# Kernel optimization log

Measured on AMD Instinct MI355X. Metric: run time of the kernel, lower is better.

Reference implementation:

```python
import jax, jax.numpy as jnp
import numpy as np

B, S, H = 2, 1024, 1024
NH, HD = 8, 128
E, TOPK, MI = 8, 2, 1024
SI = 2 * MI  # shared experts intermediate (n_shared_experts=2)
EPS = 1e-6
THETA = 10000.0


def setup_inputs() -> dict:
    key = jax.random.key(0)
    ks = jax.random.split(key, 16)
    w = lambda k, shp: (0.02 * jax.random.normal(k, shp, dtype=jnp.float32))
    # RoPE tables [S, HD]
    inv_freq = 1.0 / (THETA ** (np.arange(0, HD, 2, dtype=np.float32) / HD))
    t = np.arange(S, dtype=np.float32)
    freqs = np.outer(t, inv_freq)
    emb = np.concatenate([freqs, freqs], axis=-1)
    return {
        "hidden_states": jax.random.normal(ks[0], (B, S, H), dtype=jnp.float32),
        "ln1_w": jnp.ones((H,), jnp.float32),
        "ln2_w": jnp.ones((H,), jnp.float32),
        "q_w": w(ks[1], (H, H)),
        "k_w": w(ks[2], (H, H)),
        "v_w": w(ks[3], (H, H)),
        "o_w": w(ks[4], (H, H)),
        "cos": jnp.asarray(np.cos(emb), jnp.float32),
        "sin": jnp.asarray(np.sin(emb), jnp.float32),
        "gate_w": w(ks[5], (E, H)),
        "eg_w": w(ks[6], (E, MI, H)),
        "eu_w": w(ks[7], (E, MI, H)),
        "ed_w": w(ks[8], (E, H, MI)),
        "sg_w": w(ks[9], (SI, H)),
        "su_w": w(ks[10], (SI, H)),
        "sd_w": w(ks[11], (H, SI)),
    }


def _rmsnorm(x, w):
    return x * jax.lax.rsqrt(jnp.mean(x * x, axis=-1, keepdims=True) + EPS) * w


def _rotate_half(x):
    x1, x2 = jnp.split(x, 2, axis=-1)
    return jnp.concatenate([-x2, x1], axis=-1)


def _attention(x, q_w, k_w, v_w, o_w, cos, sin):
    b, s, h = x.shape
    q = (x @ q_w.T).reshape(b, s, NH, HD)
    k = (x @ k_w.T).reshape(b, s, NH, HD)
    v = (x @ v_w.T).reshape(b, s, NH, HD)
    c = cos[None, :s, None, :]
    sn = sin[None, :s, None, :]
    q = q * c + _rotate_half(q) * sn
    k = k * c + _rotate_half(k) * sn
    scores = jnp.einsum("bqhd,bkhd->bhqk", q, k) / jnp.sqrt(jnp.float32(HD))
    causal = jnp.tril(jnp.ones((s, s), dtype=bool))
    scores = jnp.where(causal[None, None], scores, -jnp.inf)
    p = jax.nn.softmax(scores, axis=-1)
    out = jnp.einsum("bhqk,bkhd->bqhd", p, v).reshape(b, s, h)
    return out @ o_w.T


def _mlp(x, gw, uw, dw):
    return (jax.nn.silu(x @ gw.T) * (x @ uw.T)) @ dw.T


def _moe(x, gate_w, eg_w, eu_w, ed_w, sg_w, su_w, sd_w):
    b, s, h = x.shape
    xt = x.reshape(-1, h)                              # [T, H]
    T = xt.shape[0]
    probs = jax.nn.softmax(xt @ gate_w.T, axis=-1)     # [T, E]
    rw, idx = jax.lax.top_k(probs, TOPK)               # [T, K]
    rw = rw / (jnp.sum(rw, axis=-1, keepdims=True) + 1e-20)  # norm_topk_prob
    # dense combine weights [T, E] (zero for unselected experts)
    w_full = jnp.zeros((T, E), xt.dtype).at[jnp.arange(T)[:, None], idx].add(rw)
    # dense all-expert compute, masked-combined (faithful to per-token loop math)
    g = jax.nn.silu(jnp.einsum("th,eih->tei", xt, eg_w))
    u = jnp.einsum("th,eih->tei", xt, eu_w)
    y = jnp.einsum("tei,ehi->teh", g * u, ed_w)        # [T, E, H]
    routed = jnp.einsum("teh,te->th", y, w_full)
    shared = _mlp(xt, sg_w, su_w, sd_w)
    return (routed + shared).reshape(b, s, h)


def reference(hidden_states, ln1_w, ln2_w, q_w, k_w, v_w, o_w, cos, sin,
              gate_w, eg_w, eu_w, ed_w, sg_w, su_w, sd_w):
    x = hidden_states
    x = x + _attention(_rmsnorm(x, ln1_w), q_w, k_w, v_w, o_w, cos, sin)
    x = x + _moe(_rmsnorm(x, ln2_w), gate_w, eg_w, eu_w, ed_w, sg_w, su_w, sd_w)
    return x
```

## Files before the change

kernel.cpp:

```cpp
#include <hip/hip_runtime.h>

#define B_   2
#define S_   1024
#define H_   1024
#define NH_  8
#define HD_  128
#define E_   8
#define MI_  1024
#define SI_  2048
#define T_   2048
#define CAP_ 2048

typedef unsigned short u16;
typedef __attribute__((ext_vector_type(4))) float f32x4;
typedef __attribute__((ext_vector_type(4))) unsigned short u16x4;
typedef __attribute__((ext_vector_type(8))) unsigned short u16x8;
typedef __attribute__((ext_vector_type(8))) __bf16 bf16x8;

__device__ __forceinline__ u16 f2bf(float f) {
  unsigned int u = __builtin_bit_cast(unsigned int, f);
  u = (u + 0x7fffu + ((u >> 16) & 1u)) >> 16;
  return (u16)u;
}
__device__ __forceinline__ float bf2f(u16 u) {
  return __builtin_bit_cast(float, (unsigned int)u << 16);
}
__device__ __forceinline__ float wave_sum(float v) {
#pragma unroll
  for (int o = 32; o; o >>= 1) v += __shfl_down(v, o, 64);
  return v;
}
__device__ __forceinline__ void gll16(const u16* g, u16* l) {
  __builtin_amdgcn_global_load_lds((const __attribute__((address_space(1))) void*)g,
                                   (__attribute__((address_space(3))) void*)l, 16, 0, 0);
}

__global__ void cvt_all(const float* __restrict__ q_w, const float* __restrict__ k_w,
                        const float* __restrict__ v_w, const float* __restrict__ o_w,
                        const float* __restrict__ eg_w, const float* __restrict__ eu_w,
                        const float* __restrict__ ed_w, const float* __restrict__ sg_w,
                        const float* __restrict__ su_w, const float* __restrict__ sd_w,
                        u16* __restrict__ qwb, u16* __restrict__ egu, u16* __restrict__ edb,
                        u16* __restrict__ sgu, u16* __restrict__ sdb,
                        const float* __restrict__ hidden, const float* __restrict__ ln1w,
                        u16* __restrict__ xn) {
  int bid = blockIdx.x, tid = threadIdx.x;
  if (bid >= 4352) {
    int t = bid - 4352;
    f32x4 v = ((const f32x4*)(hidden + (long)t * H_))[tid];
    float ss = v[0]*v[0] + v[1]*v[1] + v[2]*v[2] + v[3]*v[3];
    __shared__ float red[4];
    float s = wave_sum(ss);
    if ((tid & 63) == 0) red[tid >> 6] = s;
    __syncthreads();
    float r = rsqrtf((red[0] + red[1] + red[2] + red[3]) * (1.0f / H_) + 1e-6f);
    f32x4 wv = ((const f32x4*)ln1w)[tid];
    u16x4 o;
#pragma unroll
    for (int c = 0; c < 4; c++) o[c] = f2bf(v[c] * r * wv[c]);
    ((u16x4*)(xn + (long)t * H_))[tid] = o;
    return;
  }
  const float* src[8];
  u16* dst[8];
#pragma unroll
  for (int g = 0; g < 8; g++) {
    int row = bid * 8 + g;
    if (row < 4096) {
      int seg = row >> 10;
      const float* in = (seg == 0) ? q_w : (seg == 1) ? k_w : (seg == 2) ? v_w : o_w;
      src[g] = in + (long)(row & 1023) * 1024;
      dst[g] = qwb + (long)row * 1024;
    } else if (row < 20480) {
      int rel = row - 4096;
      int zu = rel >= 8192;
      int r = rel & 8191;
      int e = r >> 10, i = r & 1023;
      int orow = (i >> 4) * 32 + (i & 15) + (zu ? 16 : 0);
      src[g] = (zu ? eu_w : eg_w) + (long)r * 1024;
      dst[g] = egu + ((long)e * 2048 + orow) * 1024;
    } else if (row < 28672) {
      long f = (long)(row - 20480) * 1024;
      src[g] = ed_w + f;
      dst[g] = edb + f;
    } else if (row < 32768) {
      int rel = row - 28672;
      int zu = rel >= 2048;
      int i = rel & 2047;
      int orow = (i >> 4) * 32 + (i & 15) + (zu ? 16 : 0);
      src[g] = (zu ? su_w : sg_w) + (long)i * 1024;
      dst[g] = sgu + (long)orow * 1024;
    } else {
      long f = (long)(row - 32768) * 1024;
      src[g] = sd_w + f;
      dst[g] = sdb + f;
    }
  }
  f32x4 v[8];
#pragma unroll
  for (int g = 0; g < 8; g++)
    v[g] = __builtin_nontemporal_load((const f32x4*)src[g] + tid);
#pragma unroll
  for (int g = 0; g < 8; g++) {
    u16x4 o;
#pragma unroll
    for (int c = 0; c < 4; c++) o[c] = f2bf(v[g][c]);
    ((u16x4*)dst[g])[tid] = o;
  }
}

__global__ void rmsnorm2_gate(const float* __restrict__ x1, const float* __restrict__ ln2w,
                              const float* __restrict__ gw, u16* __restrict__ xn,
                              int* __restrict__ eidx, float* __restrict__ aw) {
  int t = blockIdx.x, tid = threadIdx.x;
  int lane = tid & 63, wave = tid >> 6;
  f32x4 v = ((const f32x4*)(x1 + (long)t * H_))[tid];
  float ss = v[0]*v[0] + v[1]*v[1] + v[2]*v[2] + v[3]*v[3];
  __shared__ float redS[4];
  __shared__ float redE[4][E_];
  float s = wave_sum(ss);
  if (lane == 0) redS[wave] = s;
  __syncthreads();
  float r = rsqrtf((redS[0] + redS[1] + redS[2] + redS[3]) * (1.0f / H_) + 1e-6f);
  f32x4 wv = ((const f32x4*)ln2w)[tid];
  float xv[4];
  u16x4 o;
#pragma unroll
  for (int c = 0; c < 4; c++) { xv[c] = v[c] * r * wv[c]; o[c] = f2bf(xv[c]); }
  ((u16x4*)(xn + (long)t * H_))[tid] = o;
  float acc[E_];
#pragma unroll
  for (int e = 0; e < E_; e++) {
    f32x4 g = ((const f32x4*)(gw + (long)e * H_))[tid];
    acc[e] = xv[0]*g[0] + xv[1]*g[1] + xv[2]*g[2] + xv[3]*g[3];
  }
#pragma unroll
  for (int e = 0; e < E_; e++) acc[e] = wave_sum(acc[e]);
  if (lane == 0)
#pragma unroll
    for (int e = 0; e < E_; e++) redE[wave][e] = acc[e];
  __syncthreads();
  if (tid == 0) {
    float l[E_];
#pragma unroll
    for (int e = 0; e < E_; e++) l[e] = redE[0][e] + redE[1][e] + redE[2][e] + redE[3][e];
    float mx = l[0];
#pragma unroll
    for (int e = 1; e < E_; e++) mx = fmaxf(mx, l[e]);
    float p[E_], z = 0.f;
#pragma unroll
    for (int e = 0; e < E_; e++) { p[e] = __expf(l[e] - mx); z += p[e]; }
    int e0 = 0;
#pragma unroll
    for (int e = 1; e < E_; e++) if (p[e] > p[e0]) e0 = e;
    int e1 = (e0 == 0) ? 1 : 0;
#pragma unroll
    for (int e = 0; e < E_; e++) if (e != e0 && p[e] > p[e1]) e1 = e;
    float q0 = p[e0] / z, q1 = p[e1] / z;
    float invs = 1.0f / (q0 + q1 + 1e-20f);
    eidx[t * 2] = e0;
    eidx[t * 2 + 1] = e1;
    aw[t * 2] = q0 * invs;
    aw[t * 2 + 1] = q1 * invs;
  }
}

__global__ __launch_bounds__(256) void route_scan(const int* __restrict__ eidx,
                                                  int* __restrict__ arow,
                                                  int* __restrict__ cursor,
                                                  int* __restrict__ itok,
                                                  int* __restrict__ wlist) {
  __shared__ int sc[E_][256];
  int tid = threadIdx.x;
  unsigned c0 = 0, c1 = 0;
  int ebuf[16];
#pragma unroll
  for (int i = 0; i < 16; i++) {
    int e = eidx[tid * 16 + i];
    ebuf[i] = e;
    if (e < 4) c0 += 1u << (8 * e); else c1 += 1u << (8 * (e - 4));
  }
#pragma unroll
  for (int e = 0; e < E_; e++)
    sc[e][tid] = (e < 4) ? (int)((c0 >> (8 * e)) & 0xff) : (int)((c1 >> (8 * (e - 4))) & 0xff);
  __syncthreads();
  for (int st = 1; st < 256; st <<= 1) {
    int v[E_];
#pragma unroll
    for (int e = 0; e < E_; e++) v[e] = (tid >= st) ? sc[e][tid - st] : 0;
    __syncthreads();
#pragma unroll
    for (int e = 0; e < E_; e++) sc[e][tid] += v[e];
    __syncthreads();
  }
  if (tid == 255) {
    int w = 0;
#pragma unroll
    for (int e = 0; e < E_; e++) {
      int cnt = sc[e][255];
      cursor[e] = cnt;
      int nt = (min(cnt, CAP_) + 127) >> 7;
      for (int mt = 0; mt < nt; mt++) wlist[w++] = (e << 8) | mt;
    }
    for (; w < 40; w++) wlist[w] = -1;
  }
  int base[E_];
#pragma unroll
  for (int e = 0; e < E_; e++) {
    int own = (e < 4) ? (int)((c0 >> (8 * e)) & 0xff) : (int)((c1 >> (8 * (e - 4))) & 0xff);
    base[e] = sc[e][tid] - own;
  }
  __syncthreads();
#pragma unroll
  for (int e = 0; e < E_; e++) sc[e][tid] = base[e];
  __syncthreads();
  unsigned r0 = 0, r1 = 0;
#pragma unroll
  for (int i = 0; i < 16; i++) {
    int e = ebuf[i];
    int run = (e < 4) ? (int)((r0 >> (8 * e)) & 0xff) : (int)((r1 >> (8 * (e - 4))) & 0xff);
    int row = e * CAP_ + sc[e][tid] + run;
    arow[tid * 16 + i] = row;
    itok[row] = (tid * 16 + i) >> 1;
    if (e < 4) r0 += 1u << (8 * e); else r1 += 1u << (8 * (e - 4));
  }
}

__global__ void rope_vtrans(const u16* __restrict__ qkvb, const float* __restrict__ cs,
                            const float* __restrict__ sn, u16* __restrict__ qb,
                            u16* __restrict__ kb, u16* __restrict__ vt) {
  int bid = blockIdx.x, tid = threadIdx.x;
  if (bid < 1024) {
    int z = bid >> 9;
    const u16* src = qkvb + (long)z * 2097152;
    u16* dstb = z ? kb : qb;
    int rb = (bid & 511) * 32 + (tid >> 3);
    int u = tid & 7;
    int h = rb & 7, bs = rb >> 3, s = bs & 1023, b = bs >> 10;
    const u16* row = src + (long)rb * 128;
    int d0 = u * 8;
    u16x8 v1 = *(const u16x8*)(row + d0);
    u16x8 v2 = *(const u16x8*)(row + d0 + 64);
    const float* c1 = cs + s * 128 + d0;
    const float* s1 = sn + s * 128 + d0;
    u16x8 o1, o2;
#pragma unroll
    for (int c = 0; c < 8; c++) {
      float a = bf2f(v1[c]), q2 = bf2f(v2[c]);
      o1[c] = f2bf(a * c1[c] - q2 * s1[c]);
      o2[c] = f2bf(q2 * c1[c + 64] + a * s1[c + 64]);
    }
    u16* orow = dstb + ((long)((b * NH_ + h) * S_ + s)) * HD_;
    *(u16x8*)(orow + d0) = o1;
    *(u16x8*)(orow + d0 + 64) = o2;
  } else {
    int vb = bid - 1024;
    int bh = vb >> 5;
    int rem = vb & 31;
    int s0 = (rem >> 1) * 64, d0 = (rem & 1) * 64;
    int b = bh >> 3, h = bh & 7;
    __shared__ u16 tile[64][68];
    const u16* vsrc = qkvb + 2 * 2097152;
#pragma unroll
    for (int it = 0; it < 4; it++) {
      int idx = it * 256 + tid;
      int r = idx >> 4, c = (idx & 15) * 4;
      u16x4 vv = *(const u16x4*)(vsrc + (((long)(b * S_ + s0 + r)) * NH_ + h) * HD_ + d0 + c);
      *(u16x4*)&tile[r][c] = vv;
    }
    __syncthreads();
#pragma unroll
    for (int it = 0; it < 4; it++) {
      int idx = it * 256 + tid;
      int dr = idx >> 4, sc = (idx & 15) * 4;
      u16x4 ov;
#pragma unroll
      for (int k = 0; k < 4; k++) ov[k] = tile[sc + k][dr];
      *(u16x4*)(vt + ((long)bh * HD_ + d0 + dr) * S_ + s0 + sc) = ov;
    }
  }
}

__global__ __launch_bounds__(256) void flash_part(
    const u16* __restrict__ qb, const u16* __restrict__ kb,
    const u16* __restrict__ vt, u16* __restrict__ Po,
    float* __restrict__ Pm, float* __restrict__ Pl) {
  int item = blockIdx.x;
  int bh = blockIdx.y;
  int qt, ch;
  if (item < 4)       { qt = item;                    ch = 0; }
  else if (item < 12) { qt = 4 + ((item - 4) >> 1);   ch = (item - 4) & 1; }
  else if (item < 24) { qt = 8 + (item - 12) / 3;     ch = (item - 12) % 3; }
  else                { qt = 12 + ((item - 24) >> 2); ch = (item - 24) & 3; }
  int j0 = ch * 4, j1 = min(j0 + 4, qt + 1);

  int tid = threadIdx.x;
  int wavei = tid >> 6, lane = tid & 63;
  int la = lane & 15, qd = lane >> 4;

  __shared__ __align__(16) u16 Ks[64 * 128];
  __shared__ __align__(16) u16 Vs[128 * 64];
  __shared__ __align__(16) u16 Ps[4][16 * 64];

  bf16x8 qf[4];
  const u16* qrow = qb + ((long)bh * S_ + qt * 64 + wavei * 16 + la) * HD_;
#pragma unroll
  for (int ks = 0; ks < 4; ks++)
    qf[ks] = *(const bf16x8*)(qrow + ks * 32 + qd * 8);

  f32x4 oacc[8];
#pragma unroll
  for (int nf = 0; nf < 8; nf++) oacc[nf] = (f32x4){0.f, 0.f, 0.f, 0.f};
  float m_i[4], l_i[4];
#pragma unroll
  for (int r = 0; r < 4; r++) { m_i[r] = -1e30f; l_i[r] = 0.f; }

  const u16* Kbase = kb + (long)bh * S_ * HD_;
  const u16* Vbase = vt + (long)bh * HD_ * S_;
  const float scale = 0.08838834764831845f;
  u16* pw = (u16*)Ps[wavei];
  int swz = la & 7;

  for (int j = j0; j < j1; j++) {
    __syncthreads();
#pragma unroll
    for (int t = 0; t < 4; t++) {
      int blk = t * 4 + wavei;
      int kr = blk * 4 + (lane >> 4);
      int kc = (lane & 15) ^ (kr & 7);
      gll16(Kbase + ((long)j * 64 + kr) * 128 + kc * 8, Ks + blk * 512);
      int vr = blk * 8 + (lane >> 3);
      int vc = (lane & 7) ^ (vr & 7);
      gll16(Vbase + (long)vr * 1024 + j * 64 + vc * 8, Vs + blk * 512);
    }
    __syncthreads();

    f32x4 sacc[4];
#pragma unroll
    for (int jf = 0; jf < 4; jf++) sacc[jf] = (f32x4){0.f, 0.f, 0.f, 0.f};
#pragma unroll
    for (int ks = 0; ks < 4; ks++)
#pragma unroll
      for (int jf = 0; jf < 4; jf++) {
        bf16x8 kfrag = *(const bf16x8*)(Ks + (jf * 16 + la) * 128 + ((ks * 4 + qd) ^ swz) * 8);
        sacc[jf] = __builtin_amdgcn_mfma_f32_16x16x32_bf16(qf[ks], kfrag, sacc[jf], 0, 0, 0);
      }

    float sv[4][4];
    int qglob = qt * 64 + wavei * 16 + qd * 4;
#pragma unroll
    for (int jf = 0; jf < 4; jf++) {
      int kglob = j * 64 + jf * 16 + la;
#pragma unroll
      for (int r = 0; r < 4; r++)
        sv[jf][r] = (kglob <= qglob + r) ? sacc[jf][r] * scale : -1e30f;
    }
    float mnew[4], alpha[4];
#pragma unroll
    for (int r = 0; r < 4; r++) {
      float mx = fmaxf(fmaxf(sv[0][r], sv[1][r]), fmaxf(sv[2][r], sv[3][r]));
#pragma unroll
      for (int o = 1; o < 16; o <<= 1) mx = fmaxf(mx, __shfl_xor(mx, o, 64));
      mnew[r] = fmaxf(m_i[r], mx);
      alpha[r] = __expf(m_i[r] - mnew[r]);
      m_i[r] = mnew[r];
    }
#pragma unroll
    for (int r = 0; r < 4; r++) {
      float sum = 0.f;
#pragma unroll
      for (int jf = 0; jf < 4; jf++) {
        float p = __expf(sv[jf][r] - mnew[r]);
        sv[jf][r] = p;
        sum += p;
      }
#pragma unroll
      for (int o = 1; o < 16; o <<= 1) sum += __shfl_xor(sum, o, 64);
      l_i[r] = l_i[r] * alpha[r] + sum;
    }
#pragma unroll
    for (int jf = 0; jf < 4; jf++)
#pragma unroll
      for (int r = 0; r < 4; r++) {
        int rp = qd * 4 + r;
        int e = jf * 16 + la;
        pw[rp * 64 + (((e >> 3) ^ (rp & 7)) << 3) + (e & 7)] = f2bf(sv[jf][r]);
      }
#pragma unroll
    for (int nf = 0; nf < 8; nf++)
#pragma unroll
      for (int r = 0; r < 4; r++) oacc[nf][r] *= alpha[r];
#pragma unroll
    for (int ks = 0; ks < 2; ks++) {
      bf16x8 pfrag = *(const bf16x8*)(pw + la * 64 + ((ks * 4 + qd) ^ swz) * 8);
#pragma unroll
      for (int nf = 0; nf < 8; nf++) {
        bf16x8 vfrag = *(const bf16x8*)(Vs + (nf * 16 + la) * 64 + (((ks * 4 + qd) & 7) ^ swz) * 8);
        oacc[nf] = __builtin_amdgcn_mfma_f32_16x16x32_bf16(pfrag, vfrag, oacc[nf], 0, 0, 0);
      }
    }
  }

  int pidx = (bh * 16 + qt) * 4 + ch;
  int rowb = wavei * 16 + qd * 4;
  u16* pob = Po + ((long)pidx * 64 + rowb) * 128;
#pragma unroll
  for (int r = 0; r < 4; r++)
#pragma unroll
    for (int nf = 0; nf < 8; nf++)
      pob[(long)r * 128 + nf * 16 + la] = f2bf(oacc[nf][r]);
  if (la == 0)
#pragma unroll
    for (int r = 0; r < 4; r++) {
      Pm[pidx * 64 + rowb + r] = m_i[r];
      Pl[pidx * 64 + rowb + r] = l_i[r];
    }
}

__global__ __launch_bounds__(256) void attn_merge(
    const u16* __restrict__ Po, const float* __restrict__ Pm,
    const float* __restrict__ Pl, u16* __restrict__ attn) {
  int qt = blockIdx.x, bh = blockIdx.y;
  int b = bh >> 3, h = bh & 7;
  int nch = (qt >> 2) + 1;
  int t = threadIdx.x;
  int row = t >> 2, cg = (t & 3) * 32;
  long base = (long)(bh * 16 + qt) * 4;
  float mv[4], wv[4];
  float M = -1e30f;
  for (int c = 0; c < nch; c++) { mv[c] = Pm[(base + c) * 64 + row]; M = fmaxf(M, mv[c]); }
  float L = 0.f;
  for (int c = 0; c < nch; c++) { wv[c] = __expf(mv[c] - M); L += wv[c] * Pl[(base + c) * 64 + row]; }
  float inv = 1.0f / L;
  f32x4 o[8];
#pragma unroll
  for (int k = 0; k < 8; k++) o[k] = (f32x4){0.f, 0.f, 0.f, 0.f};
  for (int c = 0; c < nch; c++) {
    const u16x4* src = (const u16x4*)(Po + ((base + c) * 64 + row) * 128 + cg);
#pragma unroll
    for (int k = 0; k < 8; k++) {
      u16x4 sv = src[k];
#pragma unroll
      for (int e = 0; e < 4; e++) o[k][e] += bf2f(sv[e]) * wv[c];
    }
  }
  u16* dst = attn + ((long)b * S_ + qt * 64 + row) * H_ + h * HD_ + cg;
#pragma unroll
  for (int k = 0; k < 8; k++) {
    u16x4 ov;
#pragma unroll
    for (int c = 0; c < 4; c++) ov[c] = f2bf(o[k][c] * inv);
    ((u16x4*)dst)[k] = ov;
  }
}

__global__ void final_combine(const float* __restrict__ x1, const float* __restrict__ ys,
                              const u16* __restrict__ y, const int* __restrict__ arow,
                              const float* __restrict__ aw, float* __restrict__ out) {
  int t = blockIdx.x;
  int i = threadIdx.x * 4;
  int r0 = arow[t * 2], r1 = arow[t * 2 + 1];
  float w0 = aw[t * 2], w1 = aw[t * 2 + 1];
  f32x4 a = *(const f32x4*)(x1 + (long)t * H_ + i);
  f32x4 b = *(const f32x4*)(ys + (long)t * H_ + i);
  u16x4 y0 = *(const u16x4*)(y + (long)r0 * H_ + i);
  u16x4 y1 = *(const u16x4*)(y + (long)r1 * H_ + i);
  f32x4 o;
#pragma unroll
  for (int c = 0; c < 4; c++)
    o[c] = a[c] + b[c] + w0 * bf2f(y0[c]) + w1 * bf2f(y1[c]);
  *(f32x4*)(out + (long)t * H_ + i) = o;
}

template <int MT, int STORE_BF16, int ADD_RES, int FUSE_SILU, int IND, int WL>
__global__ __launch_bounds__(256) void gemm_bt(
    const u16* __restrict__ Ag, const u16* __restrict__ Bg, void* __restrict__ Cg,
    const float* __restrict__ Res, int K, int lda, int ldb, int ldc,
    long sAz, long sBz, long sCz, const int* __restrict__ mlimit,
    const int* __restrict__ itok, const int* __restrict__ wlist) {
  constexpr int MR = MT / 32;
  int z, m0;
  if constexpr (WL) {
    int wv = wlist[blockIdx.y];
    if (wv < 0) return;
    z = wv >> 8;
    m0 = (wv & 255) * MT;
  } else {
    z = blockIdx.z;
    m0 = blockIdx.y * MT;
    if (mlimit && m0 >= mlimit[z]) return;
  }
  int n0 = blockIdx.x * 128;
  const u16* A = Ag + (IND ? 0 : z * sAz);
  const u16* B = Bg + z * sBz;
  long cbase = (long)z * sCz;

  __shared__ __align__(16) u16 As[2][MT * 64];
  __shared__ __align__(16) u16 Bs[2][128 * 64];
  int tid = threadIdx.x;
  int lane = tid & 63, wave = tid >> 6;
  int wm = (wave & 1) * (MT / 2), wn = (wave >> 1) * 64;
  int la = lane & 15, qd = lane >> 4;
  int sr = lane >> 3;
  int scs = (lane & 7) ^ (sr & 7);

  const u16* ap[MT / 32];
  const u16* bp[4];
#pragma unroll
  for (int t = 0; t < MT / 32; t++) {
    int rloc = m0 + t * 32 + wave * 8 + sr;
    long arow_g = IND ? (long)itok[(long)z * CAP_ + rloc] : (long)rloc;
    ap[t] = A + arow_g * lda + scs * 8;
  }
#pragma unroll
  for (int t = 0; t < 4; t++)
    bp[t] = B + (long)(n0 + t * 32 + wave * 8 + sr) * ldb + scs * 8;

  f32x4 acc[MR][4];
#pragma unroll
  for (int i = 0; i < MR; i++)
#pragma unroll
    for (int j = 0; j < 4; j++) acc[i][j] = (f32x4){0.f, 0.f, 0.f, 0.f};

  auto stage = [&](int buf, int k0) {
#pragma unroll
    for (int t = 0; t < MT / 32; t++)
      gll16(ap[t] + k0, &As[buf][(t * 32 + wave * 8) * 64]);
#pragma unroll
    for (int t = 0; t < 4; t++)
      gll16(bp[t] + k0, &Bs[buf][(t * 32 + wave * 8) * 64]);
  };

  int sw = la & 7;
  int nt = K >> 6;
  int cur = 0;
  stage(0, 0);
  for (int t = 0; t < nt; ++t) {
    if (t + 1 < nt) {
      stage(cur ^ 1, (t + 1) * 64);
      if constexpr (MT == 128)
        asm volatile("s_waitcnt vmcnt(8)" ::: "memory");
      else
        asm volatile("s_waitcnt vmcnt(6)" ::: "memory");
    } else {
      asm volatile("s_waitcnt vmcnt(0)" ::: "memory");
    }
    __builtin_amdgcn_s_barrier();
#pragma unroll
    for (int kk = 0; kk < 2; kk++) {
      bf16x8 af[MR], bfv[4];
#pragma unroll
      for (int i = 0; i < MR; i++)
        af[i] = *(const bf16x8*)(&As[cur][0] + (wm + i * 16 + la) * 64 + (((kk * 4 + qd) ^ sw) << 3));
#pragma unroll
      for (int j = 0; j < 4; j++)
        bfv[j] = *(const bf16x8*)(&Bs[cur][0] + (wn + j * 16 + la) * 64 + (((kk * 4 + qd) ^ sw) << 3));
#pragma unroll
      for (int i = 0; i < MR; i++)
#pragma unroll
        for (int j = 0; j < 4; j++)
          acc[i][j] = __builtin_amdgcn_mfma_f32_16x16x32_bf16(af[i], bfv[j], acc[i][j], 0, 0, 0);
    }
    __builtin_amdgcn_s_barrier();
    cur ^= 1;
  }

  if (FUSE_SILU) {
#pragma unroll
    for (int i = 0; i < MR; i++) {
#pragma unroll
      for (int jp = 0; jp < 2; jp++) {
        int hcol = ((n0 + wn) >> 1) + (jp << 4) + la;
#pragma unroll
        for (int r = 0; r < 4; r++) {
          int row = m0 + wm + i * 16 + qd * 4 + r;
          float g = acc[i][jp * 2][r], u = acc[i][jp * 2 + 1][r];
          float sg = g / (1.f + __expf(-g));
          ((u16*)Cg)[cbase + (long)row * ldc + hcol] = f2bf(sg * u);
        }
      }
    }
  } else {
#pragma unroll
    for (int i = 0; i < MR; i++) {
#pragma unroll
      for (int j = 0; j < 4; j++) {
        int col = n0 + wn + j * 16 + la;
#pragma unroll
        for (int r = 0; r < 4; r++) {
          int row = m0 + wm + i * 16 + qd * 4 + r;
          float v = acc[i][j][r];
          long ci = cbase + (long)row * ldc + col;
          if (ADD_RES) v += Res[(long)row * ldc + col];
          if (STORE_BF16) ((u16*)Cg)[ci] = f2bf(v);
          else ((float*)Cg)[ci] = v;
        }
      }
    }
  }
}

extern "C" void kernel_launch(void* const* d_in, const int* in_sizes, int n_in,
                              void* d_out, int out_size, void* d_ws, size_t ws_size,
                              hipStream_t stream) {
  const float* hidden = (const float*)d_in[0];
  const float* ln1w = (const float*)d_in[1];
  const float* ln2w = (const float*)d_in[2];
  const float* q_w = (const float*)d_in[3];
  const float* k_w = (const float*)d_in[4];
  const float* v_w = (const float*)d_in[5];
  const float* o_w = (const float*)d_in[6];
  const float* cosp = (const float*)d_in[7];
  const float* sinp = (const float*)d_in[8];
  const float* gate_w = (const float*)d_in[9];
  const float* eg_w = (const float*)d_in[10];
  const float* eu_w = (const float*)d_in[11];
  const float* ed_w = (const float*)d_in[12];
  const float* sg_w = (const float*)d_in[13];
  const float* su_w = (const float*)d_in[14];
  const float* sd_w = (const float*)d_in[15];
  float* out = (float*)d_out;

  char* w = (char*)d_ws;
  const size_t MB = 1u << 20;
  u16* qwb = (u16*)(w + 0 * MB);
  u16* egu = (u16*)(w + 8 * MB);
  u16* edb = (u16*)(w + 40 * MB);
  u16* sgu = (u16*)(w + 56 * MB);
  u16* sdb = (u16*)(w + 64 * MB);
  float* x1 = (float*)(w + 68 * MB);
  u16* xn = (u16*)(w + 76 * MB);
  u16* attn = (u16*)(w + 80 * MB);
  int* cursor = (int*)(w + 84 * MB);
  int* arow = (int*)(w + 84 * MB + 1024);
  float* aw = (float*)(w + 84 * MB + 20 * 1024);
  int* eidx = (int*)(w + 84 * MB + 40 * 1024);
  int* itok = (int*)(w + 84 * MB + 60 * 1024);
  int* wlist = (int*)(w + 84 * MB + 128 * 1024);
  u16* qkvb = (u16*)(w + 85 * MB);
  u16* qb = (u16*)(w + 109 * MB);
  u16* kb = (u16*)(w + 113 * MB);
  u16* vt = (u16*)(w + 117 * MB);
  u16* Po = (u16*)(w + 121 * MB);
  float* Pm = (float*)(w + 155 * MB);
  float* Pl = (float*)(w + 156 * MB);
  u16* hbuf = (u16*)(w + 121 * MB);
  u16* y = (u16*)(w + 157 * MB);
  u16* hs = (u16*)(w + 189 * MB);
  float* ys = (float*)(w + 197 * MB);

  const long M1 = 1048576, M2 = 2097152;

  cvt_all<<<6400, 256, 0, stream>>>(q_w, k_w, v_w, o_w, eg_w, eu_w, ed_w,
                                    sg_w, su_w, sd_w, qwb, egu, edb, sgu, sdb,
                                    hidden, ln1w, xn);

  gemm_bt<128, 1, 0, 0, 0, 0><<<dim3(8, 16, 3), 256, 0, stream>>>(
      xn, qwb, qkvb, nullptr, 1024, 1024, 1024, 1024, 0, M1, M2, nullptr, nullptr, nullptr);
  rope_vtrans<<<1536, 256, 0, stream>>>(qkvb, cosp, sinp, qb, kb, vt);
  flash_part<<<dim3(40, 16), 256, 0, stream>>>(qb, kb, vt, Po, Pm, Pl);
  attn_merge<<<dim3(16, 16), 256, 0, stream>>>(Po, Pm, Pl, attn);
  gemm_bt<64, 0, 1, 0, 0, 0><<<dim3(8, 32, 1), 256, 0, stream>>>(
      attn, qwb + 3 * M1, x1, hidden, 1024, 1024, 1024, 1024, 0, 0, 0, nullptr, nullptr, nullptr);

  rmsnorm2_gate<<<T_, 256, 0, stream>>>(x1, ln2w, gate_w, xn, eidx, aw);
  hipMemsetAsync(itok, 0, E_ * CAP_ * 4, stream);
  route_scan<<<1, 256, 0, stream>>>(eidx, arow, cursor, itok, wlist);
  gemm_bt<128, 1, 0, 1, 1, 1><<<dim3(16, 40, 1), 256, 0, stream>>>(
      xn, egu, hbuf, nullptr, 1024, 1024, 1024, MI_,
      0, (long)2 * MI_ * H_, (long)CAP_ * MI_, nullptr, itok, wlist);
  gemm_bt<128, 1, 0, 0, 0, 1><<<dim3(8, 40, 1), 256, 0, stream>>>(
      hbuf, edb, y, nullptr, 1024, 1024, 1024, 1024,
      (long)CAP_ * MI_, (long)H_ * MI_, (long)CAP_ * H_, nullptr, nullptr, wlist);
  gemm_bt<128, 1, 0, 1, 0, 0><<<dim3(32, 16, 1), 256, 0, stream>>>(
      xn, sgu, hs, nullptr, 1024, 1024, 1024, SI_, 0, 0, 0, nullptr, nullptr, nullptr);
  gemm_bt<64, 0, 0, 0, 0, 0><<<dim3(8, 32, 1), 256, 0, stream>>>(
      hs, sdb, ys, nullptr, 2048, 2048, 2048, 1024, 0, 0, 0, nullptr, nullptr, nullptr);

  final_combine<<<T_, 256, 0, stream>>>(x1, ys, y, arow, aw, out);
}
```

Measured before the change: 390.7 us.

## Overlap MoE weight conversion with flash attention and merge shared-expert GEMMs into routed launches

The MoE and shared-expert weight fp32-to-bf16 conversion moves out of the initial conversion kernel and into the flash-attention launch as extra blocks, so that conversion runs alongside attention instead of before it. The shared-expert gate/up and down GEMMs are folded into the routed-expert GEMM launches by appending work-list entries with a kind flag, which removes two kernel launches and fills idle CUs. The trade-off is extra branching and register pressure in the GEMM kernel, and possible contention between the conversion blocks and attention. The shared down projection now uses a 128-row tile instead of 64, which changes its parallelism.

Result: no change. 383.0 us (-2.0%).

```diff
diff --git a/kernel.cpp b/kernel.cpp
--- a/kernel.cpp
+++ b/kernel.cpp
@@ -35,43 +35,19 @@
                                    (__attribute__((address_space(3))) void*)l, 16, 0, 0);
 }
 
-__global__ void cvt_all(const float* __restrict__ q_w, const float* __restrict__ k_w,
-                        const float* __restrict__ v_w, const float* __restrict__ o_w,
-                        const float* __restrict__ eg_w, const float* __restrict__ eu_w,
-                        const float* __restrict__ ed_w, const float* __restrict__ sg_w,
-                        const float* __restrict__ su_w, const float* __restrict__ sd_w,
-                        u16* __restrict__ qwb, u16* __restrict__ egu, u16* __restrict__ edb,
-                        u16* __restrict__ sgu, u16* __restrict__ sdb,
-                        const float* __restrict__ hidden, const float* __restrict__ ln1w,
-                        u16* __restrict__ xn) {
-  int bid = blockIdx.x, tid = threadIdx.x;
-  if (bid >= 4352) {
-    int t = bid - 4352;
-    f32x4 v = ((const f32x4*)(hidden + (long)t * H_))[tid];
-    float ss = v[0]*v[0] + v[1]*v[1] + v[2]*v[2] + v[3]*v[3];
-    __shared__ float red[4];
-    float s = wave_sum(ss);
-    if ((tid & 63) == 0) red[tid >> 6] = s;
-    __syncthreads();
-    float r = rsqrtf((red[0] + red[1] + red[2] + red[3]) * (1.0f / H_) + 1e-6f);
-    f32x4 wv = ((const f32x4*)ln1w)[tid];
-    u16x4 o;
-#pragma unroll
-    for (int c = 0; c < 4; c++) o[c] = f2bf(v[c] * r * wv[c]);
-    ((u16x4*)(xn + (long)t * H_))[tid] = o;
-    return;
-  }
+__device__ __forceinline__ void cvt_moe_rows(
+    int row0, int tid,
+    const float* __restrict__ eg_w, const float* __restrict__ eu_w,
+    const float* __restrict__ ed_w, const float* __restrict__ sg_w,
+    const float* __restrict__ su_w, const float* __restrict__ sd_w,
+    u16* __restrict__ egu, u16* __restrict__ edb,
+    u16* __restrict__ sgu, u16* __restrict__ sdb) {
   const float* src[8];
   u16* dst[8];
 #pragma unroll
   for (int g = 0; g < 8; g++) {
-    int row = bid * 8 + g;
-    if (row < 4096) {
-      int seg = row >> 10;
-      const float* in = (seg == 0) ? q_w : (seg == 1) ? k_w : (seg == 2) ? v_w : o_w;
-      src[g] = in + (long)(row & 1023) * 1024;
-      dst[g] = qwb + (long)row * 1024;
-    } else if (row < 20480) {
+    int row = row0 + g;
+    if (row < 20480) {
       int rel = row - 4096;
       int zu = rel >= 8192;
       int r = rel & 8191;
@@ -109,6 +85,51 @@
   }
 }
 
+__global__ void cvt_all(const float* __restrict__ q_w, const float* __restrict__ k_w,
+                        const float* __restrict__ v_w, const float* __restrict__ o_w,
+                        u16* __restrict__ qwb,
+                        const float* __restrict__ hidden, const float* __restrict__ ln1w,
+                        u16* __restrict__ xn) {
+  int bid = blockIdx.x, tid = threadIdx.x;
+  if (bid >= 512) {
+    int t = bid - 512;
+    f32x4 v = ((const f32x4*)(hidden + (long)t * H_))[tid];
+    float ss = v[0]*v[0] + v[1]*v[1] + v[2]*v[2] + v[3]*v[3];
+    __shared__ float red[4];
+    float s = wave_sum(ss);
+    if ((tid & 63) == 0) red[tid >> 6] = s;
+    __syncthreads();
+    float r = rsqrtf((red[0] + red[1] + red[2] + red[3]) * (1.0f / H_) + 1e-6f);
+    f32x4 wv = ((const f32x4*)ln1w)[tid];
+    u16x4 o;
+#pragma unroll
+    for (int c = 0; c < 4; c++) o[c] = f2bf(v[c] * r * wv[c]);
+    ((u16x4*)(xn + (long)t * H_))[tid] = o;
+    return;
+  }
+  const float* src[8];
+  u16* dst[8];
+#pragma unroll
+  for (int g = 0; g < 8; g++) {
+    int row = bid * 8 + g;
+    int seg = row >> 10;
+    const float* in = (seg == 0) ? q_w : (seg == 1) ? k_w : (seg == 2) ? v_w : o_w;
+    src[g] = in + (long)(row & 1023) * 1024;
+    dst[g] = qwb + (long)row * 1024;
+  }
+  f32x4 v[8];
+#pragma unroll
+  for (int g = 0; g < 8; g++)
+    v[g] = __builtin_nontemporal_load((const f32x4*)src[g] + tid);
+#pragma unroll
+  for (int g = 0; g < 8; g++) {
+    u16x4 o;
+#pragma unroll
+    for (int c = 0; c < 4; c++) o[c] = f2bf(v[g][c]);
+    ((u16x4*)dst[g])[tid] = o;
+  }
+}
+
 __global__ void rmsnorm2_gate(const float* __restrict__ x1, const float* __restrict__ ln2w,
                               const float* __restrict__ gw, u16* __restrict__ xn,
                               int* __restrict__ eidx, float* __restrict__ aw) {
@@ -202,7 +223,8 @@
       int nt = (min(cnt, CAP_) + 127) >> 7;
       for (int mt = 0; mt < nt; mt++) wlist[w++] = (e << 8) | mt;
     }
-    for (; w < 40; w++) wlist[w] = -1;
+    for (int mt = 0; mt < 16; mt++) wlist[w++] = (1 << 16) | mt;
+    for (; w < 56; w++) wlist[w] = -1;
   }
   int base[E_];
 #pragma unroll
@@ -281,12 +303,24 @@
   }
 }
 
-__global__ __launch_bounds__(256) void flash_part(
+__global__ __launch_bounds__(256) void flash_cvt(
     const u16* __restrict__ qb, const u16* __restrict__ kb,
     const u16* __restrict__ vt, u16* __restrict__ Po,
-    float* __restrict__ Pm, float* __restrict__ Pl) {
-  int item = blockIdx.x;
-  int bh = blockIdx.y;
+    float* __restrict__ Pm, float* __restrict__ Pl,
+    const float* __restrict__ eg_w, const float* __restrict__ eu_w,
+    const float* __restrict__ ed_w, const float* __restrict__ sg_w,
+    const float* __restrict__ su_w, const float* __restrict__ sd_w,
+    u16* __restrict__ egu, u16* __restrict__ edb,
+    u16* __restrict__ sgu, u16* __restrict__ sdb) {
+  int bid = blockIdx.x;
+  int tid = threadIdx.x;
+  if (bid >= 640) {
+    int row0 = 4096 + (bid - 640) * 8;
+    cvt_moe_rows(row0, tid, eg_w, eu_w, ed_w, sg_w, su_w, sd_w, egu, edb, sgu, sdb);
+    return;
+  }
+  int item = bid % 40;
+  int bh = bid / 40;
   int qt, ch;
   if (item < 4)       { qt = item;                    ch = 0; }
   else if (item < 12) { qt = 4 + ((item - 4) >> 1);   ch = (item - 4) & 1; }
@@ -294,7 +328,6 @@
   else                { qt = 12 + ((item - 24) >> 2); ch = (item - 24) & 3; }
   int j0 = ch * 4, j1 = min(j0 + 4, qt + 1);
 
-  int tid = threadIdx.x;
   int wavei = tid >> 6, lane = tid & 63;
   int la = lane & 15, qd = lane >> 4;
 
@@ -477,23 +510,43 @@
     const u16* __restrict__ Ag, const u16* __restrict__ Bg, void* __restrict__ Cg,
     const float* __restrict__ Res, int K, int lda, int ldb, int ldc,
     long sAz, long sBz, long sCz, const int* __restrict__ mlimit,
-    const int* __restrict__ itok, const int* __restrict__ wlist) {
+    const int* __restrict__ itok, const int* __restrict__ wlist,
+    const u16* __restrict__ Ag2, const u16* __restrict__ Bg2, void* __restrict__ Cg2,
+    int lda2, int ldb2, int ldc2, int K2, int nx0, int nx1) {
   constexpr int MR = MT / 32;
-  int z, m0;
-  if constexpr (WL) {
+  int z = 0, m0, kind = 0;
+  const u16 *A, *B;
+  void* C;
+  long cbase;
+  bool ind = (IND != 0);
+  if constexpr (WL == 2) {
     int wv = wlist[blockIdx.y];
     if (wv < 0) return;
-    z = wv >> 8;
+    kind = wv >> 16;
+    if ((int)blockIdx.x >= (kind ? nx1 : nx0)) return;
     m0 = (wv & 255) * MT;
+    if (kind) {
+      A = Ag2; B = Bg2; C = Cg2;
+      lda = lda2; ldb = ldb2; ldc = ldc2; K = K2;
+      ind = false;
+      cbase = 0;
+    } else {
+      z = (wv >> 8) & 255;
+      A = Ag + (IND ? 0 : z * sAz);
+      B = Bg + z * sBz;
+      C = Cg;
+      cbase = (long)z * sCz;
+    }
   } else {
     z = blockIdx.z;
     m0 = blockIdx.y * MT;
     if (mlimit && m0 >= mlimit[z]) return;
+    A = Ag + (IND ? 0 : z * sAz);
+    B = Bg + z * sBz;
+    C = Cg;
+    cbase = (long)z * sCz;
   }
   int n0 = blockIdx.x * 128;
-  const u16* A = Ag + (IND ? 0 : z * sAz);
-  const u16* B = Bg + z * sBz;
-  long cbase = (long)z * sCz;
 
   __shared__ __align__(16) u16 As[2][MT * 64];
   __shared__ __align__(16) u16 Bs[2][128 * 64];
@@ -509,7 +562,7 @@
 #pragma unroll
   for (int t = 0; t < MT / 32; t++) {
     int rloc = m0 + t * 32 + wave * 8 + sr;
-    long arow_g = IND ? (long)itok[(long)z * CAP_ + rloc] : (long)rloc;
+    long arow_g = (IND && ind) ? (long)itok[(long)z * CAP_ + rloc] : (long)rloc;
     ap[t] = A + arow_g * lda + scs * 8;
   }
 #pragma unroll
@@ -576,11 +629,12 @@
           int row = m0 + wm + i * 16 + qd * 4 + r;
           float g = acc[i][jp * 2][r], u = acc[i][jp * 2 + 1][r];
           float sg = g / (1.f + __expf(-g));
-          ((u16*)Cg)[cbase + (long)row * ldc + hcol] = f2bf(sg * u);
+          ((u16*)C)[cbase + (long)row * ldc + hcol] = f2bf(sg * u);
         }
       }
     }
   } else {
+    bool sbf = (WL == 2) ? (kind == 0) : (STORE_BF16 != 0);
 #pragma unroll
     for (int i = 0; i < MR; i++) {
 #pragma unroll
@@ -592,8 +646,8 @@
           float v = acc[i][j][r];
           long ci = cbase + (long)row * ldc + col;
           if (ADD_RES) v += Res[(long)row * ldc + col];
-          if (STORE_BF16) ((u16*)Cg)[ci] = f2bf(v);
-          else ((float*)Cg)[ci] = v;
+          if (sbf) ((u16*)C)[ci] = f2bf(v);
+          else ((float*)C)[ci] = v;
         }
       }
     }
@@ -651,31 +705,31 @@
 
   const long M1 = 1048576, M2 = 2097152;
 
-  cvt_all<<<6400, 256, 0, stream>>>(q_w, k_w, v_w, o_w, eg_w, eu_w, ed_w,
-                                    sg_w, su_w, sd_w, qwb, egu, edb, sgu, sdb,
-                                    hidden, ln1w, xn);
+  cvt_all<<<2560, 256, 0, stream>>>(q_w, k_w, v_w, o_w, qwb, hidden, ln1w, xn);
 
   gemm_bt<128, 1, 0, 0, 0, 0><<<dim3(8, 16, 3), 256, 0, stream>>>(
-      xn, qwb, qkvb, nullptr, 1024, 1024, 1024, 1024, 0, M1, M2, nullptr, nullptr, nullptr);
+      xn, qwb, qkvb, nullptr, 1024, 1024, 1024, 1024, 0, M1, M2, nullptr, nullptr,
+      nullptr, nullptr, nullptr, nullptr, 0, 0, 0, 0, 0, 0);
   rope_vtrans<<<1536, 256, 0, stream>>>(qkvb, cosp, sinp, qb, kb, vt);
-  flash_part<<<dim3(40, 16), 256, 0, stream>>>(qb, kb, vt, Po, Pm, Pl);
+  flash_cvt<<<640 + 3840, 256, 0, stream>>>(qb, kb, vt, Po, Pm, Pl,
+                                            eg_w, eu_w, ed_w, sg_w, su_w, sd_w,
+                                            egu, edb, sgu, sdb);
   attn_merge<<<dim3(16, 16), 256, 0, stream>>>(Po, Pm, Pl, attn);
   gemm_bt<64, 0, 1, 0, 0, 0><<<dim3(8, 32, 1), 256, 0, stream>>>(
-      attn, qwb + 3 * M1, x1, hidden, 1024, 1024, 1024, 1024, 0, 0, 0, nullptr, nullptr, nullptr);
+      attn, qwb + 3 * M1, x1, hidden, 1024, 1024, 1024, 1024, 0, 0, 0, nullptr, nullptr,
+      nullptr, nullptr, nullptr, nullptr, 0, 0, 0, 0, 0, 0);
 
   rmsnorm2_gate<<<T_, 256, 0, stream>>>(x1, ln2w, gate_w, xn, eidx, aw);
   hipMemsetAsync(itok, 0, E_ * CAP_ * 4, stream);
   route_scan<<<1, 256, 0, stream>>>(eidx, arow, cursor, itok, wlist);
-  gemm_bt<128, 1, 0, 1, 1, 1><<<dim3(16, 40, 1), 256, 0, stream>>>(
+  gemm_bt<128, 1, 0, 1, 1, 2><<<dim3(32, 56, 1), 256, 0, stream>>>(
       xn, egu, hbuf, nullptr, 1024, 1024, 1024, MI_,
-      0, (long)2 * MI_ * H_, (long)CAP_ * MI_, nullptr, itok, wlist);
-  gemm_bt<128, 1, 0, 0, 0, 1><<<dim3(8, 40, 1), 256, 0, stream>>>(
+      0, (long)2 * MI_ * H_, (long)CAP_ * MI_, nullptr, itok, wlist,
+      xn, sgu, hs, 1024, 1024, SI_, 1024, 16, 32);
+  gemm_bt<128, 1, 0, 0, 0, 2><<<dim3(8, 56, 1), 256, 0, stream>>>(
       hbuf, edb, y, nullptr, 1024, 1024, 1024, 1024,
-      (long)CAP_ * MI_, (long)H_ * MI_, (long)CAP_ * H_, nullptr, nullptr, wlist);
-  gemm_bt<128, 1, 0, 1, 0, 0><<<dim3(32, 16, 1), 256, 0, stream>>>(
-      xn, sgu, hs, nullptr, 1024, 1024, 1024, SI_, 0, 0, 0, nullptr, nullptr, nullptr);
-  gemm_bt<64, 0, 0, 0, 0, 0><<<dim3(8, 32, 1), 256, 0, stream>>>(
-      hs, sdb, ys, nullptr, 2048, 2048, 2048, 1024, 0, 0, 0, nullptr, nullptr, nullptr);
+      (long)CAP_ * MI_, (long)H_ * MI_, (long)CAP_ * H_, nullptr, nullptr, wlist,
+      hs, sdb, ys, 2048, 2048, 1024, 2048, 8, 8);
 
   final_combine<<<T_, 256, 0, stream>>>(x1, ys, y, arow, aw, out);
 }
```
